# Performance work log

Measured on AMD Instinct MI355X. Metric: run time of the kernel, lower is better.

The kernel has to match this reference:

```python
import jax, jax.numpy as jnp
import numpy as np
from jax import lax

B, T, D, H, W, K, E = 2, 16, 128, 64, 64, 3, 4


def setup_inputs() -> dict:
    key = jax.random.key(0)
    ks = jax.random.split(key, 20)

    def rn(k, shape, s):
        return (jax.random.normal(k, shape) * s).astype(jnp.float32)

    D2 = 2 * D
    inp = {
        "x_re": jax.random.normal(ks[0], (B, T, D, H, W), jnp.float32),
        "x_im": jax.random.normal(ks[1], (B, T, D, H, W), jnp.float32),
        # keep dt in [0.1, 1.0] (physical timestep, avoids sqrt(0) in noise term)
        "dt": (jax.random.uniform(ks[2], (B, T)) * 0.9 + 0.1).astype(jnp.float32),
        "ln_s_g": jnp.ones((D2,), jnp.float32),
        "ln_s_b": jnp.zeros((D2,), jnp.float32),
        "ln_t_g": jnp.ones((D2,), jnp.float32),
        "ln_t_b": jnp.zeros((D2,), jnp.float32),
        "conv_metric": (1.0 + 0.02 * jax.random.normal(ks[3], (D2, H, W))).astype(jnp.float32),
        "conv_w": rn(ks[4], (D2, D2, K, K), 1.0 / np.sqrt(D2 * K * K)),
        "conv_b": jnp.zeros((D2,), jnp.float32),
        "nu": rn(ks[5], (D,), 0.5),
        "theta": rn(ks[6], (D,), 1.0),
        "enc_re": rn(ks[7], (D, D), 1.0 / np.sqrt(D)),
        "enc_im": rn(ks[8], (D, D), 1.0 / np.sqrt(D)),
        "dec_re": rn(ks[9], (D, D), 1.0 / np.sqrt(D)),
        "dec_im": rn(ks[10], (D, D), 1.0 / np.sqrt(D)),
        "src_gain": rn(ks[11], (D,), 0.1),
        "w1_re": rn(ks[12], (D, E * D), 1.0 / np.sqrt(D)),
        "w1_im": rn(ks[13], (D, E * D), 1.0 / np.sqrt(D)),
        "b1_re": jnp.zeros((E * D,), jnp.float32),
        "b1_im": jnp.zeros((E * D,), jnp.float32),
        "w2_re": rn(ks[14], (E * D, D), 1.0 / np.sqrt(E * D)),
        "w2_im": rn(ks[15], (E * D, D), 1.0 / np.sqrt(E * D)),
        "b2_re": jnp.zeros((D,), jnp.float32),
        "b2_im": jnp.zeros((D,), jnp.float32),
    }
    return inp


def _ln(x, g, b):
    m = jnp.mean(x, -1, keepdims=True)
    v = jnp.var(x, -1, keepdims=True)
    return (x - m) * lax.rsqrt(v + 1e-5) * g + b


def _cnorm(z, g, b):
    # complex LayerNorm: LN over concat(real, imag) along last dim, then re-pack
    zn = _ln(jnp.concatenate([z.real, z.imag], -1), g, b)
    r, i = jnp.split(zn, 2, -1)
    return lax.complex(r, i)


def _forward(x_re, x_im, dt, ln_s_g, ln_s_b, ln_t_g, ln_t_b, conv_metric, conv_w, conv_b,
             nu, theta, enc_re, enc_im, dec_re, dec_im, src_gain,
             w1_re, w1_im, b1_re, b1_im, w2_re, w2_im, b2_re, b2_im):
    x = lax.complex(x_re, x_im)  # [B,T,D,H,W] complex64
    Bb, Tt, Dd, Hh, Ww = x.shape
    resid = x
    # ---- spatial branch: complex LN + metric-scaled (Riemannian) Clifford conv ----
    xs = jnp.transpose(x.reshape(Bb * Tt, Dd, Hh, Ww), (0, 2, 3, 1))  # [BT,H,W,D]
    xs = jnp.transpose(_cnorm(xs, ln_s_g, ln_s_b), (0, 3, 1, 2))      # [BT,D,H,W]
    xri = jnp.concatenate([xs.real, xs.imag], 1) * conv_metric[None]  # [BT,2D,H,W]
    pad = K // 2
    oc = lax.conv_general_dilated(xri, conv_w, (1, 1), ((pad, pad), (pad, pad)),
                                  dimension_numbers=("NCHW", "OIHW", "NCHW"))
    oc = oc + conv_b[None, :, None, None]
    r, i = jnp.split(oc, 2, 1)
    x = lax.complex(r, i).reshape(Bb, Tt, Dd, Hh, Ww) + resid
    resid = x
    # ---- temporal branch: eigen-encode, source law, ZOH forcing, parallel scan ----
    xt = jnp.transpose(x, (0, 3, 4, 1, 2)).reshape(Bb * Hh * Ww, Tt, Dd)  # [N,T,D]
    xt = _cnorm(xt, ln_t_g, ln_t_b)
    dte = jnp.broadcast_to(dt[:, None, None, :], (Bb, Hh, Ww, Tt)).reshape(Bb * Hh * Ww, Tt)
    lam = lax.complex(-jax.nn.softplus(nu), theta)                 # [D], Re<0 (stable)
    op_decay = jnp.exp(lam[None, None, :] * dte[:, :, None])       # [N,T,D] complex
    op_forcing = (op_decay - 1.0) / lam                            # zero-order hold
    xe = xt @ lax.complex(enc_re, enc_im)                          # eigenbasis encode
    src = lax.complex(jnp.tanh(xe.real), jnp.tanh(xe.imag)) * src_gain
    u = (xe + src) * op_forcing
    # stochastic term (fixed key -> deterministic reference)
    nk1, nk2 = jax.random.split(jax.random.key(42))
    amp = 0.01 * jnp.sqrt(dte)[:, :, None]
    u = u + lax.complex(amp * jax.random.normal(nk1, u.shape),
                        amp * jax.random.normal(nk2, u.shape))

    def comb(c1, c2):  # h_t = a_t * h_{t-1} + u_t
        a1, u1 = c1
        a2, u2 = c2
        return a1 * a2, a2 * u1 + u2

    _, h = lax.associative_scan(comb, (op_decay, u), axis=1)       # [N,T,D]
    xo = h @ lax.complex(dec_re, dec_im)                           # eigenbasis decode
    x_drift = jnp.transpose(xo.real.reshape(Bb, Hh, Ww, Tt, Dd), (0, 3, 4, 1, 2))
    x = x_drift + resid
    # ---- complex pointwise FFN ----
    z = jnp.transpose(x, (0, 1, 3, 4, 2))                          # [B,T,H,W,D]
    hdn = z @ lax.complex(w1_re, w1_im) + lax.complex(b1_re, b1_im)
    act = lax.complex(jax.nn.gelu(hdn.real), jax.nn.gelu(hdn.imag))
    delta = act @ lax.complex(w2_re, w2_im) + lax.complex(b2_re, b2_im)
    x = x + jnp.transpose(delta, (0, 1, 4, 2, 3))
    return jnp.stack([x.real, x.imag], -1)  # [B,T,D,H,W,2] float32


def reference(x_re, x_im, dt, ln_s_g, ln_s_b, ln_t_g, ln_t_b, conv_metric, conv_w, conv_b,
              nu, theta, enc_re, enc_im, dec_re, dec_im, src_gain,
              w1_re, w1_im, b1_re, b1_im, w2_re, w2_im, b2_re, b2_im):
    return _forward(x_re, x_im, dt, ln_s_g, ln_s_b, ln_t_g, ln_t_b, conv_metric, conv_w,
                    conv_b, nu, theta, enc_re, enc_im, dec_re, dec_im, src_gain,
                    w1_re, w1_im, b1_re, b1_im, w2_re, w2_im, b2_re, b2_im)
```

## Files before the change

kernel.cpp:

```cpp
#include <hip/hip_runtime.h>
#include <hip/hip_bf16.h>
#include <stdint.h>

#define B_   2
#define T_   16
#define D_   128
#define D2_  256
#define H_   64
#define W_   64
#define HW_  4096
#define BT_  32
#define N_   8192
#define ND_  1048576
#define PLANE_ 16777216
#define WT_FLOATS 589824

typedef short bf16x8 __attribute__((ext_vector_type(8)));
typedef float f32x4 __attribute__((ext_vector_type(4)));
typedef unsigned int uint;
typedef unsigned short ushort;


__device__ __forceinline__ float softplus_f(float x) {
  return fmaxf(x, 0.0f) + log1pf(expf(-fabsf(x)));
}

__device__ __forceinline__ float gelu_fast(float x) {
  const float Ac = 2.3022082963f;
  const float Bc = 0.1029437f;
  float t = x * x;
  float z = x * fmaf(Bc, t, Ac);
  float e = __builtin_amdgcn_exp2f(z);
  float r = __builtin_amdgcn_rcpf(e + 1.0f);
  return fmaf(-x, r, x);
}

__device__ __forceinline__ float tanh_fast(float x) {
  float e = __builtin_amdgcn_exp2f(x * 2.8853900818f);
  float r = __builtin_amdgcn_rcpf(e + 1.0f);
  return fmaf(-2.0f, r, 1.0f);
}

__device__ __forceinline__ ushort f2bf(float f) {
  uint u = __float_as_uint(f);
  uint r = (u + 0x7fffu + ((u >> 16) & 1u)) >> 16;
  return (ushort)r;
}

__device__ __forceinline__ uint cvt_pk(float a, float b) {
  __hip_bfloat162 h = __float22bfloat162_rn(make_float2(a, b));
  return *reinterpret_cast<uint*>(&h);
}


__global__ __launch_bounds__(256) void k_spatial_ln(
    const float* __restrict__ x_re, const float* __restrict__ x_im,
    const float* __restrict__ g, const float* __restrict__ bb,
    const float* __restrict__ metric, ushort* __restrict__ xri,
    uint* __restrict__ xp) {
  __shared__ float vals[256][64];
  __shared__ float red1[4][64];
  __shared__ float red2[4][64];
  __shared__ float mean_s[64];
  __shared__ float rstd_s[64];
  const int blk = blockIdx.x;
  const int bt = blk >> 6;
  const int h = blk & 63;
  const int tid = threadIdx.x;
  const int w = tid & 63, q = tid >> 6;

  const float* src = (q < 2) ? x_re : x_im;
  float s1 = 0.f, s2 = 0.f;
  #pragma unroll 4
  for (int i = 0; i < 64; ++i) {
    const int c = q * 64 + i;
    const int d = c & 127;
    float v = src[((size_t)bt * D_ + d) * HW_ + h * W_ + w];
    vals[c][w] = v;
    s1 += v; s2 += v * v;
  }
  red1[q][w] = s1; red2[q][w] = s2;
  __syncthreads();
  if (tid < 64) {
    float m = red1[0][tid] + red1[1][tid] + red1[2][tid] + red1[3][tid];
    float ss = red2[0][tid] + red2[1][tid] + red2[2][tid] + red2[3][tid];
    m *= (1.f / 256.f);
    float var = ss * (1.f / 256.f) - m * m;
    mean_s[tid] = m;
    rstd_s[tid] = rsqrtf(var + 1e-5f);
  }
  __syncthreads();
  #pragma unroll
  for (int i = 0; i < 32; ++i) {
    const int d = q * 32 + i;
    xp[((size_t)bt * D_ + d) * HW_ + h * W_ + w] =
        cvt_pk(vals[d][w], vals[d + 128][w]);
  }
  const float m = mean_s[w], rs = rstd_s[w];
  const size_t ubase = (((size_t)bt * 64 + h) * 32 + q * 8) * 512 + w * 8;
  #pragma unroll
  for (int j = 0; j < 8; ++j) {
    uint4 u;
    #pragma unroll
    for (int e2 = 0; e2 < 4; ++e2) {
      const int c0 = q * 64 + j * 8 + e2 * 2;
      float v0 = (vals[c0][w] - m) * rs * g[c0] + bb[c0];
      v0 *= metric[(size_t)c0 * HW_ + h * W_ + w];
      float v1 = (vals[c0 + 1][w] - m) * rs * g[c0 + 1] + bb[c0 + 1];
      v1 *= metric[(size_t)(c0 + 1) * HW_ + h * W_ + w];
      ((uint*)&u)[e2] = cvt_pk(v0, v1);
    }
    *(uint4*)&xri[ubase + (size_t)j * 512] = u;
  }
}


__global__ __launch_bounds__(256) void k_prep_conv(
    const float* __restrict__ wg, ushort* __restrict__ cwswz) {
  const int t = blockIdx.x * 256 + threadIdx.x;
  if (t >= 73728) return;
  const int lane = t & 63;
  const int nt = (t >> 6) & 15;
  const int ks = (t >> 10) & 7;
  const int kk = t >> 13;
  const int cwv = nt >> 2, jjv = nt & 3;
  const int co_tile = (jjv < 2) ? (2 * cwv + jjv) : (8 + 2 * cwv + (jjv - 2));
  const int co = co_tile * 16 + (lane & 15);
  const int ci0 = ks * 32 + (lane >> 4) * 8;
  ushort v[8];
  #pragma unroll
  for (int e = 0; e < 8; ++e)
    v[e] = f2bf(wg[((size_t)co * 256 + ci0 + e) * 9 + kk]);
  uint4 u;
  u.x = (uint)v[0] | ((uint)v[1] << 16);
  u.y = (uint)v[2] | ((uint)v[3] << 16);
  u.z = (uint)v[4] | ((uint)v[5] << 16);
  u.w = (uint)v[6] | ((uint)v[7] << 16);
  ((uint4*)cwswz)[t] = u;
}


__global__ __launch_bounds__(512, 4) void k_conv_mfma(
    const ushort* __restrict__ xri, const ushort* __restrict__ cwswz,
    const float* __restrict__ bias,
    const uint* __restrict__ xp,
    uint* __restrict__ x2p) {
  __shared__ ushort xb[33792];
  const int tid = threadIdx.x;
  const int wave = tid >> 6, lane = tid & 63;
  const int lrow = lane & 15, lgrp = lane >> 4;
  const int blk = blockIdx.x;
  const int bt = blk >> 5;
  const int h0 = (blk & 31) * 2;
  const int cw = wave & 3;
  const int sg = wave >> 2;

  f32x4 acc[4][4];
  #pragma unroll
  for (int j = 0; j < 4; ++j)
    #pragma unroll
    for (int i = 0; i < 4; ++i) acc[j][i] = (f32x4)0.f;

  for (int half = 0; half < 2; ++half) {
    __syncthreads();
    if (tid < 128) {
      const int j = tid >> 5;
      const int u = (tid >> 1) & 15;
      const int wz = (tid & 1) * 65;
      uint4 z = {0u, 0u, 0u, 0u};
      *(uint4*)&xb[((j * 16 + u) * 66 + wz) * 8] = z;
    }
    #pragma unroll
    for (int i = 0; i < 8; ++i) {
      const int idx = i * 512 + tid;
      const int w = idx & 63;
      const int u = (idx >> 6) & 15;
      const int j = idx >> 10;
      const int hh = h0 + j - 1;
      uint4 v = {0u, 0u, 0u, 0u};
      if (hh >= 0 && hh < 64)
        v = *(const uint4*)&xri[(((size_t)bt * 64 + hh) * 32 + half * 16 + u) * 512
                                + w * 8];
      *(uint4*)&xb[((j * 16 + u) * 66 + 1 + w) * 8] = v;
    }
    __syncthreads();

    for (int kh = 0; kh < 3; ++kh) {
      for (int kw = 0; kw < 3; ++kw) {
        const int kk = kh * 3 + kw;
        #pragma unroll
        for (int ks = 0; ks < 4; ++ks) {
          bf16x8 bfr[4];
          #pragma unroll
          for (int i = 0; i < 4; ++i)
            bfr[i] = *(const bf16x8*)&xb[(((sg + kh) * 16 + ks * 4 + lgrp) * 66
                                          + i * 16 + lrow + kw) * 8];
          const int fbase = ((kk * 8 + half * 4 + ks) * 16 + cw * 4) * 64 + lane;
          #pragma unroll
          for (int j = 0; j < 4; ++j) {
            const bf16x8 afr = ((const bf16x8*)cwswz)[fbase + j * 64];
            #pragma unroll
            for (int i = 0; i < 4; ++i)
              acc[j][i] = __builtin_amdgcn_mfma_f32_16x16x32_bf16(
                  afr, bfr[i], acc[j][i], 0, 0, 0);
          }
        }
      }
    }
  }

  #pragma unroll
  for (int j = 0; j < 2; ++j) {
    #pragma unroll
    for (int jj = 0; jj < 4; ++jj) {
      const int d = (2 * cw + j) * 16 + lgrp * 4 + jj;
      const float bvr = bias[d];
      const float bvi = bias[d + 128];
      const size_t rowoff = ((size_t)bt * D_ + d) * HW_ + (h0 + sg) * W_;
      #pragma unroll
      for (int i = 0; i < 4; ++i) {
        const int w = i * 16 + lrow;
        const uint xv = xp[rowoff + w];
        const float re = acc[j][i][jj] + bvr + __uint_as_float(xv << 16);
        const float im = acc[j + 2][i][jj] + bvi + __uint_as_float(xv & 0xffff0000u);
        x2p[rowoff + w] = cvt_pk(re, im);
      }
    }
  }
}


__global__ __launch_bounds__(256) void k_prep_decay(
    const float* __restrict__ dt, const float* __restrict__ nu,
    const float* __restrict__ theta, float4* __restrict__ decay) {
  const int idx = blockIdx.x * 256 + threadIdx.x;
  const int d = idx & 127;
  const int bt = idx >> 7;
  const float dtv = dt[bt];
  const float lr = -softplus_f(nu[d]);
  const float li = theta[d];
  float s, c;
  sincosf(li * dtv, &s, &c);
  const float er = expf(lr * dtv);
  const float ar = er * c, ai = er * s;
  const float den = lr * lr + li * li;
  const float nr = ar - 1.f, ni = ai;
  float4 v;
  v.x = ar; v.y = ai;
  v.z = (nr * lr + ni * li) / den;
  v.w = (ni * lr - nr * li) / den;
  decay[idx] = v;
}


__global__ __launch_bounds__(256) void k_prep_enc(
    const float* __restrict__ enc_re, const float* __restrict__ enc_im,
    const float* __restrict__ g, ushort* __restrict__ encswz) {
  const int t = blockIdx.x * 256 + threadIdx.x;
  const int lane = t & 63;
  const int ks = (t >> 6) & 7;
  const int ntile = t >> 9;
  const int n = ntile * 16 + (lane & 15);
  const int k0 = ks * 32 + (lane >> 4) * 8;
  ushort v[8];
  #pragma unroll
  for (int e = 0; e < 8; ++e) {
    const int kp = k0 + e;
    const int k = (kp >> 1) | ((kp & 1) << 7);
    float val;
    if (k < 128) {
      val = (n < 128) ? enc_re[k * 128 + n] : enc_im[k * 128 + (n - 128)];
    } else {
      const int kk = k - 128;
      val = (n < 128) ? -enc_im[kk * 128 + n] : enc_re[kk * 128 + (n - 128)];
    }
    v[e] = f2bf(val * g[k]);
  }
  uint4 u;
  u.x = (uint)v[0] | ((uint)v[1] << 16);
  u.y = (uint)v[2] | ((uint)v[3] << 16);
  u.z = (uint)v[4] | ((uint)v[5] << 16);
  u.w = (uint)v[6] | ((uint)v[7] << 16);
  ((uint4*)encswz)[t] = u;
}

__global__ __launch_bounds__(256) void k_prep_encvec(
    const float* __restrict__ enc_re, const float* __restrict__ enc_im,
    const float* __restrict__ g, const float* __restrict__ bb,
    float* __restrict__ evec, float* __restrict__ cvec) {
  const int n = threadIdx.x;
  float se = 0.f, sc = 0.f;
  for (int k = 0; k < 256; ++k) {
    float ep;
    if (k < 128) {
      ep = (n < 128) ? enc_re[k * 128 + n] : enc_im[k * 128 + (n - 128)];
    } else {
      const int kk = k - 128;
      ep = (n < 128) ? -enc_im[kk * 128 + n] : enc_re[kk * 128 + (n - 128)];
    }
    se = fmaf(g[k], ep, se);
    sc = fmaf(bb[k], ep, sc);
  }
  evec[n] = se;
  cvec[n] = sc;
}

__global__ __launch_bounds__(256) void k_prep_dec(
    const float* __restrict__ dec_re, const float* __restrict__ dec_im,
    ushort* __restrict__ decswz) {
  const int t = blockIdx.x * 256 + threadIdx.x;
  const int lane = t & 63;
  const int ks = (t >> 6) & 7;
  const int ntile = t >> 9;
  const int n = ntile * 16 + (lane & 15);
  const int k0 = ks * 32 + (lane >> 4) * 8;
  ushort v[8];
  #pragma unroll
  for (int e = 0; e < 8; ++e) {
    const int kp = k0 + e;
    const int k = (kp >> 1) | ((kp & 1) << 7);
    float val = (k < 128) ? dec_re[k * 128 + n] : -dec_im[(k - 128) * 128 + n];
    v[e] = f2bf(val);
  }
  uint4 u;
  u.x = (uint)v[0] | ((uint)v[1] << 16);
  u.y = (uint)v[2] | ((uint)v[3] << 16);
  u.z = (uint)v[4] | ((uint)v[5] << 16);
  u.w = (uint)v[6] | ((uint)v[7] << 16);
  ((uint4*)decswz)[t] = u;
}


__global__ __launch_bounds__(256, 4) void k_temporal_mfma(
    const uint* __restrict__ x2p,
    const ushort* __restrict__ encswz,
    const float* __restrict__ evec, const float* __restrict__ cvec,
    const float4* __restrict__ decay,
    const float* __restrict__ src_gain,
    uint* __restrict__ u32) {
  __shared__ ushort xlds[64][256];
  __shared__ float red1[4][64], red2[4][64];
  __shared__ float mean_s[64], rstd_s[64];
  __shared__ float fre_s[128], fim_s[128], gain_s[128];
  const int tid = threadIdx.x;
  const int wave = tid >> 6, lane = tid & 63;
  const int lrow = lane & 15, lgrp = lane >> 4;
  const int blk = blockIdx.x;
  const int h = blk & 63;
  const int t = (blk >> 6) & 15;
  const int b = blk >> 10;
  const int bt = b * T_ + t;

  float s1 = 0.f, s2 = 0.f;
  #pragma unroll
  for (int i = 0; i < 8; ++i) {
    const int q = i * 4 + wave;
    const uint* src = &x2p[((size_t)bt * D_ + q * 4) * HW_ + h * W_ + lane];
    uint4 u;
    u.x = src[0];
    u.y = src[HW_];
    u.z = src[2 * HW_];
    u.w = src[3 * HW_];
    *(uint4*)&xlds[lane][(q ^ (lane & 7)) << 3] = u;
    #pragma unroll
    for (int e = 0; e < 4; ++e) {
      const uint v = ((const uint*)&u)[e];
      const float re = __uint_as_float(v << 16);
      const float im = __uint_as_float(v & 0xffff0000u);
      s1 += re + im;
      s2 += re * re + im * im;
    }
  }
  red1[wave][lane] = s1;
  red2[wave][lane] = s2;
  __syncthreads();
  if (tid < 64) {
    float m = red1[0][tid] + red1[1][tid] + red1[2][tid] + red1[3][tid];
    float ss = red2[0][tid] + red2[1][tid] + red2[2][tid] + red2[3][tid];
    m *= (1.f / 256.f);
    float var = ss * (1.f / 256.f) - m * m;
    mean_s[tid] = m;
    rstd_s[tid] = rsqrtf(var + 1e-5f);
  }
  if (tid < 128) {
    const float4 dc = decay[bt * 128 + tid];
    fre_s[tid] = dc.z;
    fim_s[tid] = dc.w;
    gain_s[tid] = src_gain[tid];
  }
  __syncthreads();

  f32x4 acc[4][4];
  #pragma unroll
  for (int ntl = 0; ntl < 4; ++ntl)
    #pragma unroll
    for (int st = 0; st < 4; ++st) acc[ntl][st] = (f32x4)0.f;

  const int swz = lrow & 7;
  const int ntb[4] = {wave * 2, wave * 2 + 1, wave * 2 + 8, wave * 2 + 9};
  #pragma unroll
  for (int ks = 0; ks < 8; ++ks) {
    bf16x8 bfr[4];
    #pragma unroll
    for (int st = 0; st < 4; ++st)
      bfr[st] = *(const bf16x8*)&xlds[st * 16 + lrow][(((ks * 4 + lgrp) ^ swz)) << 3];
    #pragma unroll
    for (int ntl = 0; ntl < 4; ++ntl) {
      const bf16x8 afr = ((const bf16x8*)encswz)[(ntb[ntl] * 8 + ks) * 64 + lane];
      #pragma unroll
      for (int st = 0; st < 4; ++st)
        acc[ntl][st] = __builtin_amdgcn_mfma_f32_16x16x32_bf16(
            afr, bfr[st], acc[ntl][st], 0, 0, 0);
    }
  }

  const int nbase = (b * 64 + h) * 64;
  #pragma unroll
  for (int ntl = 0; ntl < 2; ++ntl) {
    const int d0 = ntb[ntl] * 16 + lgrp * 4;
    #pragma unroll
    for (int st = 0; st < 4; ++st) {
      const int site = st * 16 + lrow;
      const float m = mean_s[site], rs = rstd_s[site];
      #pragma unroll
      for (int j = 0; j < 4; ++j) {
        const int d = d0 + j;
        const float xer = rs * acc[ntl][st][j] - rs * m * evec[d] + cvec[d];
        const float xei = rs * acc[ntl + 2][st][j] - rs * m * evec[d + 128] + cvec[d + 128];
        const float sr = tanh_fast(xer) * gain_s[d];
        const float si = tanh_fast(xei) * gain_s[d];
        const float vr = xer + sr, vi = xei + si;
        const float ur = vr * fre_s[d] - vi * fim_s[d];
        const float ui = vr * fim_s[d] + vi * fre_s[d];
        u32[(size_t)t * ND_ + (size_t)d * N_ + nbase + site] = cvt_pk(ur, ui);
      }
    }
  }
}


__global__ __launch_bounds__(256) void k_scan(
    uint* __restrict__ u32, const float4* __restrict__ decay) {
  const int idx = blockIdx.x * 256 + threadIdx.x;
  const int n = idx & 8191;
  const int d = idx >> 13;
  const int b = n >> 12;
  float hr = 0.f, hi = 0.f;
  #pragma unroll
  for (int t = 0; t < 16; ++t) {
    const float4 dc = decay[(b * 16 + t) * 128 + d];
    const size_t off = (size_t)t * ND_ + idx;
    const uint v = u32[off];
    const float ur = __uint_as_float(v << 16);
    const float ui = __uint_as_float(v & 0xffff0000u);
    const float nr = fmaf(dc.x, hr, fmaf(-dc.y, hi, ur));
    const float ni = fmaf(dc.x, hi, fmaf(dc.y, hr, ui));
    hr = nr; hi = ni;
    u32[off] = cvt_pk(hr, hi);
  }
}


__global__ __launch_bounds__(256) void k_prep_b1(
    const float* __restrict__ w1_re, const float* __restrict__ w1_im,
    ushort* __restrict__ b1swz) {
  const int t = blockIdx.x * 256 + threadIdx.x;
  const int lane = t & 63;
  const int ks = (t >> 6) & 7;
  const int ntile = t >> 9;
  const int n = ntile * 16 + (lane & 15);
  const int k0 = ks * 32 + (lane >> 4) * 8;
  ushort v[8];
  #pragma unroll
  for (int e = 0; e < 8; ++e) {
    const int kp = k0 + e;
    const int k = (kp >> 1) | ((kp & 1) << 7);
    float val;
    if (k < 128) {
      val = (n < 512) ? w1_re[k * 512 + n] : w1_im[k * 512 + (n - 512)];
    } else {
      const int kk = k - 128;
      val = (n < 512) ? -w1_im[kk * 512 + n] : w1_re[kk * 512 + (n - 512)];
    }
    v[e] = f2bf(val);
  }
  uint4 u;
  u.x = (uint)v[0] | ((uint)v[1] << 16);
  u.y = (uint)v[2] | ((uint)v[3] << 16);
  u.z = (uint)v[4] | ((uint)v[5] << 16);
  u.w = (uint)v[6] | ((uint)v[7] << 16);
  ((uint4*)b1swz)[t] = u;
}

__global__ __launch_bounds__(256) void k_prep_b2(
    const float* __restrict__ w2_re, const float* __restrict__ w2_im,
    ushort* __restrict__ b2swz) {
  const int t = blockIdx.x * 256 + threadIdx.x;
  const int lane = t & 63;
  const int kc = (t >> 6) & 31;
  const int rowtile = t >> 11;
  const int n2 = rowtile * 16 + (lane & 15);
  const int k0 = kc * 32 + (lane >> 4) * 8;
  ushort v[8];
  #pragma unroll
  for (int e = 0; e < 8; ++e) {
    const int k = k0 + e;
    float val;
    if (k < 512) {
      val = (n2 < 128) ? w2_re[k * 128 + n2] : w2_im[k * 128 + (n2 - 128)];
    } else {
      const int kk = k - 512;
      val = (n2 < 128) ? -w2_im[kk * 128 + n2] : w2_re[kk * 128 + (n2 - 128)];
    }
    v[e] = f2bf(val);
  }
  uint4 u;
  u.x = (uint)v[0] | ((uint)v[1] << 16);
  u.y = (uint)v[2] | ((uint)v[3] << 16);
  u.z = (uint)v[4] | ((uint)v[5] << 16);
  u.w = (uint)v[6] | ((uint)v[7] << 16);
  ((uint4*)b2swz)[t] = u;
}


__global__ __launch_bounds__(256, 2) void k_ffn_mfma(
    const uint* __restrict__ x2p, const uint* __restrict__ h32,
    const ushort* __restrict__ decswz,
    const ushort* __restrict__ b1swz, const ushort* __restrict__ b2swz,
    const float* __restrict__ b1_re, const float* __restrict__ b1_im,
    const float* __restrict__ b2_re, const float* __restrict__ b2_im,
    float* __restrict__ out) {
  __shared__ ushort xlds[64][256];
  __shared__ ushort actlds[2][64][136];
  const int tid = threadIdx.x;
  const int wave = tid >> 6, lane = tid & 63;
  const int lrow = lane & 15, lgrp = lane >> 4;
  const int blk = blockIdx.x;
  const int bt = blk >> 6;
  const int hrow = blk & 63;
  const int hw0 = hrow * 64;
  const int b = bt >> 4, t = bt & 15;
  const int nbase = (b * 64 + hrow) * 64;
  const bf16x8* b1f = (const bf16x8*)b1swz;
  const bf16x8* b2f = (const bf16x8*)b2swz;
  const bf16x8* dcf = (const bf16x8*)decswz;
  ushort* hbuf = &actlds[0][0][0];

  #pragma unroll
  for (int i = 0; i < 8; ++i) {
    const int q = i * 4 + wave;
    const uint* src = &x2p[((size_t)bt * D_ + q * 4) * HW_ + hw0 + lane];
    uint4 u;
    u.x = src[0]; u.y = src[HW_]; u.z = src[2 * HW_]; u.w = src[3 * HW_];
    *(uint4*)&xlds[lane][(q ^ (lane & 7)) << 3] = u;
  }
  #pragma unroll
  for (int i = 0; i < 8; ++i) {
    const int q = i * 4 + wave;
    const size_t o = (size_t)t * ND_ + (size_t)(q * 4) * N_ + nbase + lane;
    uint4 u;
    u.x = h32[o]; u.y = h32[o + N_]; u.z = h32[o + 2 * N_]; u.w = h32[o + 3 * N_];
    *(uint4*)&hbuf[lane * 264 + ((q ^ (lane & 7)) << 3)] = u;
  }

  bf16x8 a1[2][8];
  #pragma unroll
  for (int ntl = 0; ntl < 2; ++ntl)
    #pragma unroll
    for (int ks = 0; ks < 8; ++ks)
      a1[ntl][ks] = b1f[((wave * 2 + ntl) * 8 + ks) * 64 + lane];
  bf16x8 a2[4][2];
  #pragma unroll
  for (int rt = 0; rt < 4; ++rt)
    #pragma unroll
    for (int k2 = 0; k2 < 2; ++k2)
      a2[rt][k2] = b2f[((wave * 4 + rt) * 32 + k2) * 64 + lane];

  __syncthreads();
  const int swz = lrow & 7;

  {
    f32x4 dr[2][4];
    #pragma unroll
    for (int ntl = 0; ntl < 2; ++ntl)
      #pragma unroll
      for (int st = 0; st < 4; ++st) dr[ntl][st] = (f32x4)0.f;
    #pragma unroll
    for (int ks = 0; ks < 8; ++ks) {
      bf16x8 bfr[4];
      #pragma unroll
      for (int st = 0; st < 4; ++st)
        bfr[st] = *(const bf16x8*)&hbuf[(st * 16 + lrow) * 264
                                        + (((ks * 4 + lgrp) ^ swz) << 3)];
      #pragma unroll
      for (int ntl = 0; ntl < 2; ++ntl) {
        const bf16x8 afr = dcf[((wave * 2 + ntl) * 8 + ks) * 64 + lane];
        #pragma unroll
        for (int st = 0; st < 4; ++st)
          dr[ntl][st] = __builtin_amdgcn_mfma_f32_16x16x32_bf16(
              afr, bfr[st], dr[ntl][st], 0, 0, 0);
      }
    }
    #pragma unroll
    for (int ntl = 0; ntl < 2; ++ntl) {
      #pragma unroll
      for (int st = 0; st < 4; ++st) {
        const int site = st * 16 + lrow;
        #pragma unroll
        for (int j = 0; j < 4; ++j) {
          const int d = (wave * 2 + ntl) * 16 + lgrp * 4 + j;
          ushort* p = &xlds[site][(((d >> 2) ^ (site & 7)) << 3) + (d & 3) * 2];
          const uint v = *(uint*)p;
          const float re = __uint_as_float(v << 16) + dr[ntl][st][j];
          *(uint*)p = (v & 0xffff0000u) | (uint)f2bf(re);
        }
      }
    }
  }
  __syncthreads();

  f32x4 dacc[4][4];
  #pragma unroll
  for (int rt = 0; rt < 4; ++rt)
    #pragma unroll
    for (int st = 0; st < 4; ++st) dacc[rt][st] = (f32x4)0.f;

  for (int chunk = 0; chunk < 8; ++chunk) {
    const int nc = (chunk + 1) & 7;

    f32x4 hacc[2][4];
    #pragma unroll
    for (int ntl = 0; ntl < 2; ++ntl)
      #pragma unroll
      for (int st = 0; st < 4; ++st) hacc[ntl][st] = (f32x4)0.f;

    #pragma unroll
    for (int ks = 0; ks < 8; ++ks) {
      bf16x8 bfr[4];
      #pragma unroll
      for (int st = 0; st < 4; ++st)
        bfr[st] = *(const bf16x8*)&xlds[st * 16 + lrow][(((ks * 4 + lgrp) ^ swz)) << 3];
      #pragma unroll
      for (int ntl = 0; ntl < 2; ++ntl)
        #pragma unroll
        for (int st = 0; st < 4; ++st)
          hacc[ntl][st] = __builtin_amdgcn_mfma_f32_16x16x32_bf16(
              a1[ntl][ks], bfr[st], hacc[ntl][st], 0, 0, 0);
    }

    #pragma unroll
    for (int ntl = 0; ntl < 2; ++ntl)
      #pragma unroll
      for (int ks = 0; ks < 8; ++ks)
        a1[ntl][ks] = b1f[((nc * 8 + wave * 2 + ntl) * 8 + ks) * 64 + lane];

    uint* act32 = (uint*)&actlds[chunk & 1][0][0];
    #pragma unroll
    for (int ntl = 0; ntl < 2; ++ntl) {
      const int nlocal0 = (wave * 2 + ntl) * 16 + lgrp * 4;
      const int ng0 = chunk * 128 + nlocal0;
      #pragma unroll
      for (int st = 0; st < 4; ++st) {
        float gv[4];
        #pragma unroll
        for (int j = 0; j < 4; ++j) {
          const int ng = ng0 + j;
          const float bias = (ng < 512) ? b1_re[ng] : b1_im[ng - 512];
          gv[j] = gelu_fast(hacc[ntl][st][j] + bias);
        }
        const int site = st * 16 + lrow;
        act32[site * 68 + (nlocal0 >> 1)] = cvt_pk(gv[0], gv[1]);
        act32[site * 68 + (nlocal0 >> 1) + 1] = cvt_pk(gv[2], gv[3]);
      }
    }

    bf16x8 a2b[4][2];
    #pragma unroll
    for (int rt = 0; rt < 4; ++rt)
      #pragma unroll
      for (int k2 = 0; k2 < 2; ++k2)
        a2b[rt][k2] = b2f[((wave * 4 + rt) * 32 + chunk * 4 + 2 + k2) * 64 + lane];

    __syncthreads();

    const ushort* actb = &actlds[chunk & 1][0][0];
    #pragma unroll
    for (int ks2 = 0; ks2 < 2; ++ks2) {
      bf16x8 bfr[4];
      #pragma unroll
      for (int st = 0; st < 4; ++st)
        bfr[st] = *(const bf16x8*)&actb[(st * 16 + lrow) * 136 + ks2 * 32 + lgrp * 8];
      #pragma unroll
      for (int rt = 0; rt < 4; ++rt)
        #pragma unroll
        for (int st = 0; st < 4; ++st)
          dacc[rt][st] = __builtin_amdgcn_mfma_f32_16x16x32_bf16(
              a2[rt][ks2], bfr[st], dacc[rt][st], 0, 0, 0);
    }
    #pragma unroll
    for (int ks2 = 0; ks2 < 2; ++ks2) {
      bf16x8 bfr[4];
      #pragma unroll
      for (int st = 0; st < 4; ++st)
        bfr[st] = *(const bf16x8*)&actb[(st * 16 + lrow) * 136 + (ks2 + 2) * 32 + lgrp * 8];
      #pragma unroll
      for (int rt = 0; rt < 4; ++rt)
        #pragma unroll
        for (int st = 0; st < 4; ++st)
          dacc[rt][st] = __builtin_amdgcn_mfma_f32_16x16x32_bf16(
              a2b[rt][ks2], bfr[st], dacc[rt][st], 0, 0, 0);
    }

    #pragma unroll
    for (int rt = 0; rt < 4; ++rt)
      #pragma unroll
      for (int k2 = 0; k2 < 2; ++k2)
        a2[rt][k2] = b2f[((wave * 4 + rt) * 32 + nc * 4 + k2) * 64 + lane];
  }

  #pragma unroll
  for (int rt = 0; rt < 4; ++rt) {
    #pragma unroll
    for (int j = 0; j < 4; ++j) {
      const int n2 = (wave * 4 + rt) * 16 + lgrp * 4 + j;
      const int d = n2 & 127;
      const int c = n2 >> 7;
      const float bias2 = c ? b2_im[d] : b2_re[d];
      #pragma unroll
      for (int st = 0; st < 4; ++st) {
        const int site = st * 16 + lrow;
        const uint pr = *(const uint*)&xlds[site][(((d >> 2) ^ (site & 7)) << 3)
                                                  + (d & 3) * 2];
        const float rv = c ? __uint_as_float(pr & 0xffff0000u)
                           : __uint_as_float(pr << 16);
        const size_t idx = (size_t)(bt * D_ + d) * HW_ + hw0 + site;
        out[idx * 2 + c] = rv + dacc[rt][st][j] + bias2;
      }
    }
  }
}


extern "C" void kernel_launch(void* const* d_in, const int* in_sizes, int n_in,
                              void* d_out, int out_size, void* d_ws, size_t ws_size,
                              hipStream_t stream) {
  const float* x_re   = (const float*)d_in[0];
  const float* x_im   = (const float*)d_in[1];
  const float* dt     = (const float*)d_in[2];
  const float* ln_s_g = (const float*)d_in[3];
  const float* ln_s_b = (const float*)d_in[4];
  const float* ln_t_g = (const float*)d_in[5];
  const float* ln_t_b = (const float*)d_in[6];
  const float* metric = (const float*)d_in[7];
  const float* conv_w = (const float*)d_in[8];
  const float* conv_b = (const float*)d_in[9];
  const float* nu     = (const float*)d_in[10];
  const float* theta  = (const float*)d_in[11];
  const float* enc_re = (const float*)d_in[12];
  const float* enc_im = (const float*)d_in[13];
  const float* dec_re = (const float*)d_in[14];
  const float* dec_im = (const float*)d_in[15];
  const float* src_g  = (const float*)d_in[16];
  const float* w1_re  = (const float*)d_in[17];
  const float* w1_im  = (const float*)d_in[18];
  const float* b1_re  = (const float*)d_in[19];
  const float* b1_im  = (const float*)d_in[20];
  const float* w2_re  = (const float*)d_in[21];
  const float* w2_im  = (const float*)d_in[22];
  const float* b2_re  = (const float*)d_in[23];
  const float* b2_im  = (const float*)d_in[24];
  float* out = (float*)d_out;
  float* ws = (float*)d_ws;

  float* wt   = ws;
  float* bufA = ws + WT_FLOATS;
  ushort* wt16  = (ushort*)wt;
  ushort* cwswz = wt16;
  ushort* b1swz = wt16;
  ushort* b2swz = wt16 + 262144;
  ushort* encswz = wt16 + 524288;
  ushort* decswz = wt16 + 589824;
  float*  evec   = (float*)(wt16 + 622592);
  float*  cvec   = evec + 256;
  float4* decay  = (float4*)(cvec + 256);
  ushort* xri_bf = (ushort*)bufA;

  const size_t needA = ((size_t)WT_FLOATS + 3 * (size_t)PLANE_) * 4 + (2u << 20);
  const bool planA = ws_size >= needA;
  uint *u32p, *x2p, *xp;
  float* ffn_out;
  if (planA) {
    u32p = (uint*)bufA + 32768;
    x2p  = (uint*)bufA + PLANE_ + 65536;
    xp   = (uint*)bufA + 2 * (size_t)PLANE_ + 131072;
    ffn_out = out;
  } else {
    u32p = (uint*)out;
    x2p  = (uint*)out + PLANE_;
    xp   = (uint*)bufA + PLANE_;
    ffn_out = bufA;
  }

  k_prep_conv<<<288, 256, 0, stream>>>(conv_w, cwswz);
  k_prep_decay<<<16, 256, 0, stream>>>(dt, nu, theta, decay);
  k_spatial_ln<<<BT_ * H_, 256, 0, stream>>>(x_re, x_im, ln_s_g, ln_s_b, metric,
                                             xri_bf, xp);
  k_conv_mfma<<<BT_ * 32, 512, 0, stream>>>(xri_bf, cwswz, conv_b, xp, x2p);
  k_prep_b1<<<128, 256, 0, stream>>>(w1_re, w1_im, b1swz);
  k_prep_b2<<<128, 256, 0, stream>>>(w2_re, w2_im, b2swz);
  k_prep_enc<<<32, 256, 0, stream>>>(enc_re, enc_im, ln_t_g, encswz);
  k_prep_encvec<<<1, 256, 0, stream>>>(enc_re, enc_im, ln_t_g, ln_t_b, evec, cvec);
  k_prep_dec<<<16, 256, 0, stream>>>(dec_re, dec_im, decswz);
  k_temporal_mfma<<<B_ * T_ * H_, 256, 0, stream>>>(x2p, encswz, evec, cvec,
                                                    decay, src_g, u32p);
  k_scan<<<ND_ / 256, 256, 0, stream>>>(u32p, decay);
  k_ffn_mfma<<<BT_ * H_, 256, 0, stream>>>(x2p, u32p, decswz, b1swz, b2swz,
                                           b1_re, b1_im, b2_re, b2_im, ffn_out);
  if (!planA) {
    hipMemcpyAsync(d_out, ffn_out, (size_t)2 * PLANE_ * sizeof(float),
                   hipMemcpyDeviceToDevice, stream);
  }
}
```

Baseline: 665.5 us.

## Merge weight-prep kernels into one launch, widen scan loads, relax temporal launch bounds

Folds seven small weight/decay preprocessing kernels into a single block-range-dispatched kernel, using a non-aliased workspace layout so the conv and FFN weight buffers no longer overlap. The scan kernel now processes two adjacent channels-positions per thread using 64-bit loads and stores, halving the grid. The temporal kernel's launch_bounds occupancy hint drops from 4 to 2 blocks, letting the compiler use more registers. Together these aim to cut launch overhead and memory transaction count, at the cost of a slightly larger workspace and possibly lower occupancy in the temporal kernel.

```diff
diff --git a/kernel.cpp b/kernel.cpp
--- a/kernel.cpp
+++ b/kernel.cpp
@@ -13,7 +13,7 @@
 #define N_   8192
 #define ND_  1048576
 #define PLANE_ 16777216
-#define WT_FLOATS 589824
+#define PREP_FLOATS 655360
 
 typedef short bf16x8 __attribute__((ext_vector_type(8)));
 typedef float f32x4 __attribute__((ext_vector_type(4)));
@@ -50,6 +50,166 @@
 __device__ __forceinline__ uint cvt_pk(float a, float b) {
   __hip_bfloat162 h = __float22bfloat162_rn(make_float2(a, b));
   return *reinterpret_cast<uint*>(&h);
+}
+
+__device__ __forceinline__ uint4 pack8(const ushort v[8]) {
+  uint4 u;
+  u.x = (uint)v[0] | ((uint)v[1] << 16);
+  u.y = (uint)v[2] | ((uint)v[3] << 16);
+  u.z = (uint)v[4] | ((uint)v[5] << 16);
+  u.w = (uint)v[6] | ((uint)v[7] << 16);
+  return u;
+}
+
+
+__global__ __launch_bounds__(256) void k_prep_all(
+    const float* __restrict__ wg,
+    const float* __restrict__ dt, const float* __restrict__ nu,
+    const float* __restrict__ theta,
+    const float* __restrict__ w1_re, const float* __restrict__ w1_im,
+    const float* __restrict__ w2_re, const float* __restrict__ w2_im,
+    const float* __restrict__ enc_re, const float* __restrict__ enc_im,
+    const float* __restrict__ dec_re, const float* __restrict__ dec_im,
+    const float* __restrict__ g, const float* __restrict__ bb,
+    ushort* __restrict__ cwswz, float4* __restrict__ decay,
+    ushort* __restrict__ b1swz, ushort* __restrict__ b2swz,
+    ushort* __restrict__ encswz, ushort* __restrict__ decswz,
+    float* __restrict__ evec, float* __restrict__ cvec) {
+  const int blk = blockIdx.x;
+  const int tid = threadIdx.x;
+
+  if (blk < 288) {
+    const int t = blk * 256 + tid;
+    if (t >= 73728) return;
+    const int lane = t & 63;
+    const int nt = (t >> 6) & 15;
+    const int ks = (t >> 10) & 7;
+    const int kk = t >> 13;
+    const int cwv = nt >> 2, jjv = nt & 3;
+    const int co_tile = (jjv < 2) ? (2 * cwv + jjv) : (8 + 2 * cwv + (jjv - 2));
+    const int co = co_tile * 16 + (lane & 15);
+    const int ci0 = ks * 32 + (lane >> 4) * 8;
+    ushort v[8];
+    #pragma unroll
+    for (int e = 0; e < 8; ++e)
+      v[e] = f2bf(wg[((size_t)co * 256 + ci0 + e) * 9 + kk]);
+    ((uint4*)cwswz)[t] = pack8(v);
+  } else if (blk < 304) {
+    const int idx = (blk - 288) * 256 + tid;
+    const int d = idx & 127;
+    const int bt = idx >> 7;
+    const float dtv = dt[bt];
+    const float lr = -softplus_f(nu[d]);
+    const float li = theta[d];
+    float s, c;
+    sincosf(li * dtv, &s, &c);
+    const float er = expf(lr * dtv);
+    const float ar = er * c, ai = er * s;
+    const float den = lr * lr + li * li;
+    const float nr = ar - 1.f, ni = ai;
+    float4 v;
+    v.x = ar; v.y = ai;
+    v.z = (nr * lr + ni * li) / den;
+    v.w = (ni * lr - nr * li) / den;
+    decay[idx] = v;
+  } else if (blk < 432) {
+    const int t = (blk - 304) * 256 + tid;
+    const int lane = t & 63;
+    const int ks = (t >> 6) & 7;
+    const int ntile = t >> 9;
+    const int n = ntile * 16 + (lane & 15);
+    const int k0 = ks * 32 + (lane >> 4) * 8;
+    ushort v[8];
+    #pragma unroll
+    for (int e = 0; e < 8; ++e) {
+      const int kp = k0 + e;
+      const int k = (kp >> 1) | ((kp & 1) << 7);
+      float val;
+      if (k < 128) {
+        val = (n < 512) ? w1_re[k * 512 + n] : w1_im[k * 512 + (n - 512)];
+      } else {
+        const int kk = k - 128;
+        val = (n < 512) ? -w1_im[kk * 512 + n] : w1_re[kk * 512 + (n - 512)];
+      }
+      v[e] = f2bf(val);
+    }
+    ((uint4*)b1swz)[t] = pack8(v);
+  } else if (blk < 560) {
+    const int t = (blk - 432) * 256 + tid;
+    const int lane = t & 63;
+    const int kc = (t >> 6) & 31;
+    const int rowtile = t >> 11;
+    const int n2 = rowtile * 16 + (lane & 15);
+    const int k0 = kc * 32 + (lane >> 4) * 8;
+    ushort v[8];
+    #pragma unroll
+    for (int e = 0; e < 8; ++e) {
+      const int k = k0 + e;
+      float val;
+      if (k < 512) {
+        val = (n2 < 128) ? w2_re[k * 128 + n2] : w2_im[k * 128 + (n2 - 128)];
+      } else {
+        const int kk = k - 512;
+        val = (n2 < 128) ? -w2_im[kk * 128 + n2] : w2_re[kk * 128 + (n2 - 128)];
+      }
+      v[e] = f2bf(val);
+    }
+    ((uint4*)b2swz)[t] = pack8(v);
+  } else if (blk < 592) {
+    const int t = (blk - 560) * 256 + tid;
+    const int lane = t & 63;
+    const int ks = (t >> 6) & 7;
+    const int ntile = t >> 9;
+    const int n = ntile * 16 + (lane & 15);
+    const int k0 = ks * 32 + (lane >> 4) * 8;
+    ushort v[8];
+    #pragma unroll
+    for (int e = 0; e < 8; ++e) {
+      const int kp = k0 + e;
+      const int k = (kp >> 1) | ((kp & 1) << 7);
+      float val;
+      if (k < 128) {
+        val = (n < 128) ? enc_re[k * 128 + n] : enc_im[k * 128 + (n - 128)];
+      } else {
+        const int kk = k - 128;
+        val = (n < 128) ? -enc_im[kk * 128 + n] : enc_re[kk * 128 + (n - 128)];
+      }
+      v[e] = f2bf(val * g[k]);
+    }
+    ((uint4*)encswz)[t] = pack8(v);
+  } else if (blk < 593) {
+    const int n = tid;
+    float se = 0.f, sc = 0.f;
+    for (int k = 0; k < 256; ++k) {
+      float ep;
+      if (k < 128) {
+        ep = (n < 128) ? enc_re[k * 128 + n] : enc_im[k * 128 + (n - 128)];
+      } else {
+        const int kk = k - 128;
+        ep = (n < 128) ? -enc_im[kk * 128 + n] : enc_re[kk * 128 + (n - 128)];
+      }
+      se = fmaf(g[k], ep, se);
+      sc = fmaf(bb[k], ep, sc);
+    }
+    evec[n] = se;
+    cvec[n] = sc;
+  } else {
+    const int t = (blk - 593) * 256 + tid;
+    const int lane = t & 63;
+    const int ks = (t >> 6) & 7;
+    const int ntile = t >> 9;
+    const int n = ntile * 16 + (lane & 15);
+    const int k0 = ks * 32 + (lane >> 4) * 8;
+    ushort v[8];
+    #pragma unroll
+    for (int e = 0; e < 8; ++e) {
+      const int kp = k0 + e;
+      const int k = (kp >> 1) | ((kp & 1) << 7);
+      float val = (k < 128) ? dec_re[k * 128 + n] : -dec_im[(k - 128) * 128 + n];
+      v[e] = f2bf(val);
+    }
+    ((uint4*)decswz)[t] = pack8(v);
+  }
 }
 
 
@@ -112,31 +272,6 @@
     }
     *(uint4*)&xri[ubase + (size_t)j * 512] = u;
   }
-}
-
-
-__global__ __launch_bounds__(256) void k_prep_conv(
-    const float* __restrict__ wg, ushort* __restrict__ cwswz) {
-  const int t = blockIdx.x * 256 + threadIdx.x;
-  if (t >= 73728) return;
-  const int lane = t & 63;
-  const int nt = (t >> 6) & 15;
-  const int ks = (t >> 10) & 7;
-  const int kk = t >> 13;
-  const int cwv = nt >> 2, jjv = nt & 3;
-  const int co_tile = (jjv < 2) ? (2 * cwv + jjv) : (8 + 2 * cwv + (jjv - 2));
-  const int co = co_tile * 16 + (lane & 15);
-  const int ci0 = ks * 32 + (lane >> 4) * 8;
-  ushort v[8];
-  #pragma unroll
-  for (int e = 0; e < 8; ++e)
-    v[e] = f2bf(wg[((size_t)co * 256 + ci0 + e) * 9 + kk]);
-  uint4 u;
-  u.x = (uint)v[0] | ((uint)v[1] << 16);
-  u.y = (uint)v[2] | ((uint)v[3] << 16);
-  u.z = (uint)v[4] | ((uint)v[5] << 16);
-  u.w = (uint)v[6] | ((uint)v[7] << 16);
-  ((uint4*)cwswz)[t] = u;
 }
 
 
@@ -230,108 +365,7 @@
 }
 
 
-__global__ __launch_bounds__(256) void k_prep_decay(
-    const float* __restrict__ dt, const float* __restrict__ nu,
-    const float* __restrict__ theta, float4* __restrict__ decay) {
-  const int idx = blockIdx.x * 256 + threadIdx.x;
-  const int d = idx & 127;
-  const int bt = idx >> 7;
-  const float dtv = dt[bt];
-  const float lr = -softplus_f(nu[d]);
-  const float li = theta[d];
-  float s, c;
-  sincosf(li * dtv, &s, &c);
-  const float er = expf(lr * dtv);
-  const float ar = er * c, ai = er * s;
-  const float den = lr * lr + li * li;
-  const float nr = ar - 1.f, ni = ai;
-  float4 v;
-  v.x = ar; v.y = ai;
-  v.z = (nr * lr + ni * li) / den;
-  v.w = (ni * lr - nr * li) / den;
-  decay[idx] = v;
-}
-
-
-__global__ __launch_bounds__(256) void k_prep_enc(
-    const float* __restrict__ enc_re, const float* __restrict__ enc_im,
-    const float* __restrict__ g, ushort* __restrict__ encswz) {
-  const int t = blockIdx.x * 256 + threadIdx.x;
-  const int lane = t & 63;
-  const int ks = (t >> 6) & 7;
-  const int ntile = t >> 9;
-  const int n = ntile * 16 + (lane & 15);
-  const int k0 = ks * 32 + (lane >> 4) * 8;
-  ushort v[8];
-  #pragma unroll
-  for (int e = 0; e < 8; ++e) {
-    const int kp = k0 + e;
-    const int k = (kp >> 1) | ((kp & 1) << 7);
-    float val;
-    if (k < 128) {
-      val = (n < 128) ? enc_re[k * 128 + n] : enc_im[k * 128 + (n - 128)];
-    } else {
-      const int kk = k - 128;
-      val = (n < 128) ? -enc_im[kk * 128 + n] : enc_re[kk * 128 + (n - 128)];
-    }
-    v[e] = f2bf(val * g[k]);
-  }
-  uint4 u;
-  u.x = (uint)v[0] | ((uint)v[1] << 16);
-  u.y = (uint)v[2] | ((uint)v[3] << 16);
-  u.z = (uint)v[4] | ((uint)v[5] << 16);
-  u.w = (uint)v[6] | ((uint)v[7] << 16);
-  ((uint4*)encswz)[t] = u;
-}
-
-__global__ __launch_bounds__(256) void k_prep_encvec(
-    const float* __restrict__ enc_re, const float* __restrict__ enc_im,
-    const float* __restrict__ g, const float* __restrict__ bb,
-    float* __restrict__ evec, float* __restrict__ cvec) {
-  const int n = threadIdx.x;
-  float se = 0.f, sc = 0.f;
-  for (int k = 0; k < 256; ++k) {
-    float ep;
-    if (k < 128) {
-      ep = (n < 128) ? enc_re[k * 128 + n] : enc_im[k * 128 + (n - 128)];
-    } else {
-      const int kk = k - 128;
-      ep = (n < 128) ? -enc_im[kk * 128 + n] : enc_re[kk * 128 + (n - 128)];
-    }
-    se = fmaf(g[k], ep, se);
-    sc = fmaf(bb[k], ep, sc);
-  }
-  evec[n] = se;
-  cvec[n] = sc;
-}
-
-__global__ __launch_bounds__(256) void k_prep_dec(
-    const float* __restrict__ dec_re, const float* __restrict__ dec_im,
-    ushort* __restrict__ decswz) {
-  const int t = blockIdx.x * 256 + threadIdx.x;
-  const int lane = t & 63;
-  const int ks = (t >> 6) & 7;
-  const int ntile = t >> 9;
-  const int n = ntile * 16 + (lane & 15);
-  const int k0 = ks * 32 + (lane >> 4) * 8;
-  ushort v[8];
-  #pragma unroll
-  for (int e = 0; e < 8; ++e) {
-    const int kp = k0 + e;
-    const int k = (kp >> 1) | ((kp & 1) << 7);
-    float val = (k < 128) ? dec_re[k * 128 + n] : -dec_im[(k - 128) * 128 + n];
-    v[e] = f2bf(val);
-  }
-  uint4 u;
-  u.x = (uint)v[0] | ((uint)v[1] << 16);
-  u.y = (uint)v[2] | ((uint)v[3] << 16);
-  u.z = (uint)v[4] | ((uint)v[5] << 16);
-  u.w = (uint)v[6] | ((uint)v[7] << 16);
-  ((uint4*)decswz)[t] = u;
-}
-
-
-__global__ __launch_bounds__(256, 4) void k_temporal_mfma(
+__global__ __launch_bounds__(256, 2) void k_temporal_mfma(
     const uint* __restrict__ x2p,
     const ushort* __restrict__ encswz,
     const float* __restrict__ evec, const float* __restrict__ cvec,
@@ -440,86 +474,36 @@
 
 
 __global__ __launch_bounds__(256) void k_scan(
-    uint* __restrict__ u32, const float4* __restrict__ decay) {
-  const int idx = blockIdx.x * 256 + threadIdx.x;
-  const int n = idx & 8191;
-  const int d = idx >> 13;
+    uint2* __restrict__ u64p, const float4* __restrict__ decay) {
+  const int gidx = blockIdx.x * 256 + threadIdx.x;
+  const int flat = gidx * 2;
+  const int n = flat & 8191;
+  const int d = flat >> 13;
   const int b = n >> 12;
-  float hr = 0.f, hi = 0.f;
+  float h0r = 0.f, h0i = 0.f, h1r = 0.f, h1i = 0.f;
   #pragma unroll
   for (int t = 0; t < 16; ++t) {
     const float4 dc = decay[(b * 16 + t) * 128 + d];
-    const size_t off = (size_t)t * ND_ + idx;
-    const uint v = u32[off];
-    const float ur = __uint_as_float(v << 16);
-    const float ui = __uint_as_float(v & 0xffff0000u);
-    const float nr = fmaf(dc.x, hr, fmaf(-dc.y, hi, ur));
-    const float ni = fmaf(dc.x, hi, fmaf(dc.y, hr, ui));
-    hr = nr; hi = ni;
-    u32[off] = cvt_pk(hr, hi);
-  }
-}
-
-
-__global__ __launch_bounds__(256) void k_prep_b1(
-    const float* __restrict__ w1_re, const float* __restrict__ w1_im,
-    ushort* __restrict__ b1swz) {
-  const int t = blockIdx.x * 256 + threadIdx.x;
-  const int lane = t & 63;
-  const int ks = (t >> 6) & 7;
-  const int ntile = t >> 9;
-  const int n = ntile * 16 + (lane & 15);
-  const int k0 = ks * 32 + (lane >> 4) * 8;
-  ushort v[8];
-  #pragma unroll
-  for (int e = 0; e < 8; ++e) {
-    const int kp = k0 + e;
-    const int k = (kp >> 1) | ((kp & 1) << 7);
-    float val;
-    if (k < 128) {
-      val = (n < 512) ? w1_re[k * 512 + n] : w1_im[k * 512 + (n - 512)];
-    } else {
-      const int kk = k - 128;
-      val = (n < 512) ? -w1_im[kk * 512 + n] : w1_re[kk * 512 + (n - 512)];
-    }
-    v[e] = f2bf(val);
-  }
-  uint4 u;
-  u.x = (uint)v[0] | ((uint)v[1] << 16);
-  u.y = (uint)v[2] | ((uint)v[3] << 16);
-  u.z = (uint)v[4] | ((uint)v[5] << 16);
-  u.w = (uint)v[6] | ((uint)v[7] << 16);
-  ((uint4*)b1swz)[t] = u;
-}
-
-__global__ __launch_bounds__(256) void k_prep_b2(
-    const float* __restrict__ w2_re, const float* __restrict__ w2_im,
-    ushort* __restrict__ b2swz) {
-  const int t = blockIdx.x * 256 + threadIdx.x;
-  const int lane = t & 63;
-  const int kc = (t >> 6) & 31;
-  const int rowtile = t >> 11;
-  const int n2 = rowtile * 16 + (lane & 15);
-  const int k0 = kc * 32 + (lane >> 4) * 8;
-  ushort v[8];
-  #pragma unroll
-  for (int e = 0; e < 8; ++e) {
-    const int k = k0 + e;
-    float val;
-    if (k < 512) {
-      val = (n2 < 128) ? w2_re[k * 128 + n2] : w2_im[k * 128 + (n2 - 128)];
-    } else {
-      const int kk = k - 512;
-      val = (n2 < 128) ? -w2_im[kk * 128 + n2] : w2_re[kk * 128 + (n2 - 128)];
-    }
-    v[e] = f2bf(val);
-  }
-  uint4 u;
-  u.x = (uint)v[0] | ((uint)v[1] << 16);
-  u.y = (uint)v[2] | ((uint)v[3] << 16);
-  u.z = (uint)v[4] | ((uint)v[5] << 16);
-  u.w = (uint)v[6] | ((uint)v[7] << 16);
-  ((uint4*)b2swz)[t] = u;
+    const size_t off = ((size_t)t * ND_ + flat) >> 1;
+    uint2 v = u64p[off];
+    {
+      const float ur = __uint_as_float(v.x << 16);
+      const float ui = __uint_as_float(v.x & 0xffff0000u);
+      const float nr = fmaf(dc.x, h0r, fmaf(-dc.y, h0i, ur));
+      const float ni = fmaf(dc.x, h0i, fmaf(dc.y, h0r, ui));
+      h0r = nr; h0i = ni;
+      v.x = cvt_pk(h0r, h0i);
+    }
+    {
+      const float ur = __uint_as_float(v.y << 16);
+      const float ui = __uint_as_float(v.y & 0xffff0000u);
+      const float nr = fmaf(dc.x, h1r, fmaf(-dc.y, h1i, ur));
+      const float ni = fmaf(dc.x, h1i, fmaf(dc.y, h1r, ui));
+      h1r = nr; h1i = ni;
+      v.y = cvt_pk(h1r, h1i);
+    }
+    u64p[off] = v;
+  }
 }
 
 
@@ -772,20 +756,19 @@
   float* out = (float*)d_out;
   float* ws = (float*)d_ws;
 
-  float* wt   = ws;
-  float* bufA = ws + WT_FLOATS;
-  ushort* wt16  = (ushort*)wt;
-  ushort* cwswz = wt16;
-  ushort* b1swz = wt16;
-  ushort* b2swz = wt16 + 262144;
-  ushort* encswz = wt16 + 524288;
-  ushort* decswz = wt16 + 589824;
-  float*  evec   = (float*)(wt16 + 622592);
+  ushort* wt16   = (ushort*)ws;
+  ushort* cwswz  = wt16;
+  ushort* b1swz  = wt16 + 589824;
+  ushort* b2swz  = wt16 + 851968;
+  ushort* encswz = wt16 + 1114112;
+  ushort* decswz = wt16 + 1179648;
+  float*  evec   = (float*)(wt16 + 1212416);
   float*  cvec   = evec + 256;
   float4* decay  = (float4*)(cvec + 256);
+  float*  bufA   = ws + PREP_FLOATS;
   ushort* xri_bf = (ushort*)bufA;
 
-  const size_t needA = ((size_t)WT_FLOATS + 3 * (size_t)PLANE_) * 4 + (2u << 20);
+  const size_t needA = ((size_t)PREP_FLOATS + 3 * (size_t)PLANE_) * 4 + (2u << 20);
   const bool planA = ws_size >= needA;
   uint *u32p, *x2p, *xp;
   float* ffn_out;
@@ -801,19 +784,17 @@
     ffn_out = bufA;
   }
 
-  k_prep_conv<<<288, 256, 0, stream>>>(conv_w, cwswz);
-  k_prep_decay<<<16, 256, 0, stream>>>(dt, nu, theta, decay);
+  k_prep_all<<<609, 256, 0, stream>>>(conv_w, dt, nu, theta, w1_re, w1_im,
+                                      w2_re, w2_im, enc_re, enc_im, dec_re, dec_im,
+                                      ln_t_g, ln_t_b,
+                                      cwswz, decay, b1swz, b2swz, encswz, decswz,
+                                      evec, cvec);
   k_spatial_ln<<<BT_ * H_, 256, 0, stream>>>(x_re, x_im, ln_s_g, ln_s_b, metric,
                                              xri_bf, xp);
   k_conv_mfma<<<BT_ * 32, 512, 0, stream>>>(xri_bf, cwswz, conv_b, xp, x2p);
-  k_prep_b1<<<128, 256, 0, stream>>>(w1_re, w1_im, b1swz);
-  k_prep_b2<<<128, 256, 0, stream>>>(w2_re, w2_im, b2swz);
-  k_prep_enc<<<32, 256, 0, stream>>>(enc_re, enc_im, ln_t_g, encswz);
-  k_prep_encvec<<<1, 256, 0, stream>>>(enc_re, enc_im, ln_t_g, ln_t_b, evec, cvec);
-  k_prep_dec<<<16, 256, 0, stream>>>(dec_re, dec_im, decswz);
   k_temporal_mfma<<<B_ * T_ * H_, 256, 0, stream>>>(x2p, encswz, evec, cvec,
                                                     decay, src_g, u32p);
-  k_scan<<<ND_ / 256, 256, 0, stream>>>(u32p, decay);
+  k_scan<<<ND_ / 512, 256, 0, stream>>>((uint2*)u32p, decay);
   k_ffn_mfma<<<BT_ * H_, 256, 0, stream>>>(x2p, u32p, decswz, b1swz, b2swz,
                                            b1_re, b1_im, b2_re, b2_im, ffn_out);
   if (!planA) {
```

Result: no change. 657.8 us (-1.2%).
